# Optimization experiments

Hardware: AMD Instinct MI355X
Metric: run time of the kernel (lower is better)

## Reference

```python
import jax, jax.numpy as jnp
import numpy as np

B, S, H = 2, 2048, 1024
NH, HD = 16, 64
WINDOW = 1024
ROPE_THETA = 10000.0
MAX_POS = 2048


def _rope_tables(dtype=jnp.float32):
    # RotaryEmbedding cache: inv_freq over even dims, emb = cat(freqs, freqs)
    inv_freq = 1.0 / (ROPE_THETA ** (jnp.arange(0, HD, 2, dtype=jnp.float32) / HD))
    t = jnp.arange(MAX_POS, dtype=jnp.float32)
    freqs = jnp.einsum('i,j->ij', t, inv_freq)          # [MAX_POS, HD//2]
    emb = jnp.concatenate([freqs, freqs], axis=-1)      # [MAX_POS, HD]
    return jnp.cos(emb).astype(dtype), jnp.sin(emb).astype(dtype)


def _rotate_half(x):
    x1, x2 = x[..., : HD // 2], x[..., HD // 2:]
    return jnp.concatenate([-x2, x1], axis=-1)


def setup_inputs() -> dict:
    key = jax.random.key(0)
    ks = jax.random.split(key, 5)
    sc = 0.02
    hidden_states = jax.random.normal(ks[0], (B, S, H), dtype=jnp.float32)
    position_ids = jnp.tile(jnp.arange(S, dtype=jnp.int64)[None, :], (B, 1))
    wq = jax.random.normal(ks[1], (H, H), dtype=jnp.float32) * sc
    wk = jax.random.normal(ks[2], (H, H), dtype=jnp.float32) * sc
    wv = jax.random.normal(ks[3], (H, H), dtype=jnp.float32) * sc
    wo = jax.random.normal(ks[4], (H, H), dtype=jnp.float32) * sc
    zeros = jnp.zeros((H,), dtype=jnp.float32)
    return {"hidden_states": hidden_states, "position_ids": position_ids,
            "wq": wq, "bq": zeros, "wk": wk, "bk": zeros,
            "wv": wv, "bv": zeros, "wo": wo, "bo": zeros}


def reference(hidden_states, position_ids, wq, bq, wk, bk, wv, bv, wo, bo):
    b, s, _ = hidden_states.shape
    # projections (nn.Linear: x @ W.T + b), split heads -> [B, NH, S, HD]
    def proj(w, bias):
        y = hidden_states @ w.T + bias
        return y.reshape(b, s, NH, HD).transpose(0, 2, 1, 3)
    q, k, v = proj(wq, bq), proj(wk, bk), proj(wv, bv)

    # RoPE: gather cos/sin at position_ids, broadcast over heads
    cos_t, sin_t = _rope_tables(hidden_states.dtype)
    pos = jnp.clip(position_ids, 0, MAX_POS - 1)
    cos = cos_t[pos][:, None, :, :]   # [B, 1, S, HD]
    sin = sin_t[pos][:, None, :, :]
    q = q * cos + _rotate_half(q) * sin
    k = k * cos + _rotate_half(k) * sin

    # scaled dot-product attention with causal + sliding-window band mask
    scores = jnp.einsum('bhqd,bhkd->bhqk', q, k) / jnp.sqrt(jnp.asarray(HD, hidden_states.dtype))
    i = jnp.arange(s)[:, None]
    j = jnp.arange(s)[None, :]
    allowed = (j <= i) & (i - j < WINDOW)          # banded causal mask [S, S]
    neg = jnp.asarray(jnp.finfo(hidden_states.dtype).min, hidden_states.dtype)
    scores = jnp.where(allowed[None, None, :, :], scores, neg)
    probs = jax.nn.softmax(scores, axis=-1)
    ctx = jnp.einsum('bhqk,bhkd->bhqd', probs, v)  # [B, NH, S, HD]
    ctx = ctx.transpose(0, 2, 1, 3).reshape(b, s, H)
    return ctx @ wo.T + bo
```

## Files before the change

kernel.cpp:

```cpp
#include <hip/hip_runtime.h>

#define BATCH 2
#define SDIM 2048
#define HDIM 1024
#define NHEADS 16
#define HEADD 64
#define WIN 1024

typedef __bf16 bf16x8 __attribute__((ext_vector_type(8)));
typedef __bf16 bf16x4 __attribute__((ext_vector_type(4)));
typedef float f32x4 __attribute__((ext_vector_type(4)));
typedef unsigned short u16x8 __attribute__((ext_vector_type(8)));

__device__ __forceinline__ unsigned short bf16_rne(float f) {
    union { float f; unsigned u; } x; x.f = f;
    unsigned r = x.u + 0x7fffu + ((x.u >> 16) & 1u);
    return (unsigned short)(r >> 16);
}

__device__ __forceinline__ void gload_lds16(const unsigned short* g, unsigned short* l) {
    __builtin_amdgcn_global_load_lds(
        (const __attribute__((address_space(1))) void*)g,
        (__attribute__((address_space(3))) void*)l, 16, 0, 0);
}

__global__ __launch_bounds__(256) void prep_kernel(
    const float* __restrict__ hs, const float* __restrict__ wq, const float* __restrict__ wk,
    const float* __restrict__ wv, const float* __restrict__ wo,
    unsigned short* __restrict__ Xb, unsigned short* __restrict__ Wqkv,
    unsigned short* __restrict__ Wob, float2* __restrict__ cstab)
{
    int i = blockIdx.x * 256 + threadIdx.x;
    if (i < 2097152) {
        const float* src; unsigned short* dst; int off;
        if (i < 1048576)      { src = hs; dst = Xb;             off = i; }
        else if (i < 1310720) { src = wq; dst = Wqkv;           off = i - 1048576; }
        else if (i < 1572864) { src = wk; dst = Wqkv + 1048576; off = i - 1310720; }
        else if (i < 1835008) { src = wv; dst = Wqkv + 2097152; off = i - 1572864; }
        else                  { src = wo; dst = Wob;            off = i - 1835008; }
        float4 v = reinterpret_cast<const float4*>(src)[off];
        ushort4 r;
        r.x = bf16_rne(v.x); r.y = bf16_rne(v.y); r.z = bf16_rne(v.z); r.w = bf16_rne(v.w);
        reinterpret_cast<ushort4*>(dst)[off] = r;
    } else {
        int j = i - 2097152;
        int p = j >> 5, f = j & 31;
        float inv = (float)pow(10000.0, -(double)f / 32.0);
        float ang = (float)p * inv;
        cstab[j] = make_float2(cosf(ang), sinf(ang));
    }
}

__global__ __launch_bounds__(256) void vtrans_kernel(
    const unsigned short* __restrict__ in, unsigned short* __restrict__ out)
{
    __shared__ __align__(16) unsigned short T[64 * 72];
    int s0 = blockIdx.x * 64, h = blockIdx.y, b = blockIdx.z;
    long hb = (long)(b * NHEADS + h) * SDIM * HEADD;
    int t = threadIdx.x;
    int sr = t >> 2, sc = (t & 3) * 16;
    u16x8 v0 = *(const u16x8*)&in[hb + (long)(s0 + sr) * HEADD + sc];
    u16x8 v1 = *(const u16x8*)&in[hb + (long)(s0 + sr) * HEADD + sc + 8];
    #pragma unroll
    for (int j = 0; j < 8; j++) {
        T[(sc + j) * 72     + (sr ^ (sc & 48))] = (unsigned short)v0[j];
        T[(sc + 8 + j) * 72 + (sr ^ (sc & 48))] = (unsigned short)v1[j];
    }
    __syncthreads();
    int dr = t >> 2, dc = (t & 3) * 16;
    int cb = dc ^ (dr & 48);
    u16x8 o0 = *(const u16x8*)&T[dr * 72 + cb];
    u16x8 o1 = *(const u16x8*)&T[dr * 72 + cb + 8];
    *(u16x8*)&out[hb + (long)dr * SDIM + s0 + dc]     = o0;
    *(u16x8*)&out[hb + (long)dr * SDIM + s0 + dc + 8] = o1;
}

__device__ __forceinline__ void mfma_gemm_128(
    const unsigned short* __restrict__ A,
    const unsigned short* __restrict__ Bm,
    int m0, int n0, int tid,
    unsigned short* lA, unsigned short* lB,
    f32x4 acc[4][4])
{
    const int K = 1024;
    const int BUF = 128 * 32;
    int lane = tid & 63, wid = tid >> 6;
    int wm = wid >> 1, wn = wid & 1;
    int lane15 = lane & 15, lhi = lane >> 4;
    int lrow = lane >> 2;
    int swz = (lane & 3) ^ ((lane >> 3) & 3);
    const unsigned short* ga0 = A  + (long)(m0 + wid * 32      + lrow) * K + swz * 8;
    const unsigned short* ga1 = A  + (long)(m0 + wid * 32 + 16 + lrow) * K + swz * 8;
    const unsigned short* gb0 = Bm + (long)(n0 + wid * 32      + lrow) * K + swz * 8;
    const unsigned short* gb1 = Bm + (long)(n0 + wid * 32 + 16 + lrow) * K + swz * 8;
    unsigned short* la0 = lA + (wid * 32)      * 32;
    unsigned short* la1 = lA + (wid * 32 + 16) * 32;
    unsigned short* lb0 = lB + (wid * 32)      * 32;
    unsigned short* lb1 = lB + (wid * 32 + 16) * 32;
    int ru = (lhi ^ ((lane15 >> 1) & 3)) * 8;

#define STAGE_G(boff, kt) \
    gload_lds16(ga0 + (kt) * 32, la0 + (boff)); \
    gload_lds16(ga1 + (kt) * 32, la1 + (boff)); \
    gload_lds16(gb0 + (kt) * 32, lb0 + (boff)); \
    gload_lds16(gb1 + (kt) * 32, lb1 + (boff));

#define COMPUTE_G(off) { \
    bf16x8 af[4], bfr[4]; \
    _Pragma("unroll") \
    for (int f = 0; f < 4; f++) { \
        af[f]  = *(const bf16x8*)&lA[(off) + (wm * 64 + f * 16 + lane15) * 32 + ru]; \
        bfr[f] = *(const bf16x8*)&lB[(off) + (wn * 64 + f * 16 + lane15) * 32 + ru]; \
    } \
    _Pragma("unroll") \
    for (int i = 0; i < 4; i++) \
        _Pragma("unroll") \
        for (int j = 0; j < 4; j++) \
            acc[i][j] = __builtin_amdgcn_mfma_f32_16x16x32_bf16(af[i], bfr[j], acc[i][j], 0, 0, 0); \
}

#define WAITB(n) \
    asm volatile("s_waitcnt vmcnt(" #n ")" ::: "memory"); \
    __builtin_amdgcn_s_barrier(); \
    asm volatile("" ::: "memory");

    STAGE_G(0, 0);
    STAGE_G(BUF, 1);
    #pragma unroll 1
    for (int t = 0; t < 30; t += 3) {
        WAITB(4);
        STAGE_G(2 * BUF, t + 2);
        COMPUTE_G(0);
        WAITB(4);
        STAGE_G(0, t + 3);
        COMPUTE_G(BUF);
        WAITB(4);
        STAGE_G(BUF, t + 4);
        COMPUTE_G(2 * BUF);
    }
    WAITB(4);
    COMPUTE_G(0);
    WAITB(0);
    COMPUTE_G(BUF);

#undef STAGE_G
#undef COMPUTE_G
#undef WAITB
}

__global__ __launch_bounds__(256) void gemm_qkv_kernel(
    const unsigned short* __restrict__ Xb,
    const unsigned short* __restrict__ Wb,
    const float* __restrict__ bq, const float* __restrict__ bk, const float* __restrict__ bv,
    const float2* __restrict__ cstab,
    unsigned short* __restrict__ qbuf, unsigned short* __restrict__ kbuf, unsigned short* __restrict__ vbuf)
{
    __shared__ __align__(16) unsigned short lA[3 * 128 * 32];
    __shared__ __align__(16) unsigned short lB[3 * 128 * 32];
    int tid = threadIdx.x;
    int lane = tid & 63, wid = tid >> 6;
    int wm = wid >> 1, wn = wid & 1;
    int lane15 = lane & 15, lhi = lane >> 4;
    int m0 = blockIdx.y * 128, n0 = blockIdx.x * 128;
    f32x4 acc[4][4];
    #pragma unroll
    for (int i = 0; i < 4; i++)
        #pragma unroll
        for (int j = 0; j < 4; j++)
            acc[i][j] = (f32x4){0.f, 0.f, 0.f, 0.f};

    mfma_gemm_128(Xb, Wb, m0, n0, tid, lA, lB, acc);

    int proj = n0 >> 10;
    int ncol0 = (n0 & 1023) + wn * 64;
    int h = ncol0 >> 6;
    unsigned short* dst = proj == 0 ? qbuf : (proj == 1 ? kbuf : vbuf);
    const float* bias = proj == 0 ? bq : (proj == 1 ? bk : bv);
    #pragma unroll
    for (int fm = 0; fm < 4; fm++) {
        #pragma unroll
        for (int reg = 0; reg < 4; reg++) {
            int m = m0 + wm * 64 + fm * 16 + lhi * 4 + reg;
            int bb = m >> 11, s = m & (SDIM - 1);
            long base = ((long)(bb * NHEADS + h) * SDIM + s) * HEADD;
            if (proj < 2) {
                #pragma unroll
                for (int fn = 0; fn < 2; fn++) {
                    int j = fn * 16 + lane15;
                    float lo = acc[fm][fn][reg]     + bias[ncol0 + j];
                    float hi = acc[fm][fn + 2][reg] + bias[ncol0 + 32 + j];
                    float2 cs = cstab[s * 32 + j];
                    float rl = lo * cs.x - hi * cs.y;
                    float rh = hi * cs.x + lo * cs.y;
                    if (proj == 0) { rl *= 0.125f; rh *= 0.125f; }
                    dst[base + j]      = bf16_rne(rl);
                    dst[base + 32 + j] = bf16_rne(rh);
                }
            } else {
                #pragma unroll
                for (int fn = 0; fn < 4; fn++) {
                    int d = fn * 16 + lane15;
                    dst[base + d] = bf16_rne(acc[fm][fn][reg] + bias[ncol0 + d]);
                }
            }
        }
    }
}

__global__ __launch_bounds__(256) void attn_kernel(
    const unsigned short* __restrict__ qb,
    const unsigned short* __restrict__ kbf,
    const unsigned short* __restrict__ vtb,
    unsigned short* __restrict__ ctxb)
{
    __shared__ __align__(16) unsigned short Kl[64 * 72];
    __shared__ __align__(16) unsigned short Vl[64 * 72];
    __shared__ __align__(16) unsigned short Pl[4][16 * 72];
    int tid = threadIdx.x, lane = tid & 63, wid = tid >> 6;
    int lane15 = lane & 15, lhi = lane >> 4;

    int slot = blockIdx.x;
    int xcd = slot & 7;
    int pos = slot >> 3;
    int hbg = pos >> 5;
    int hb32 = xcd + 8 * hbg;
    int h = hb32 & 15, b = hb32 >> 4;
    int qt = 31 - (pos & 31);
    int q0b = qt * 64;
    int qw = q0b + wid * 16;

    long hb = (long)(b * NHEADS + h) * SDIM * HEADD;
    const unsigned short* qptr = qb + hb;
    const unsigned short* kptr = kbf + hb;
    const unsigned short* vt   = vtb + hb;
    unsigned short* Pw = Pl[wid];

    bf16x8 aq0 = *(const bf16x8*)&qptr[(qw + lane15) * HEADD + lhi * 8];
    bf16x8 aq1 = *(const bf16x8*)&qptr[(qw + lane15) * HEADD + 32 + lhi * 8];

    f32x4 acc[4];
    #pragma unroll
    for (int f = 0; f < 4; f++) acc[f] = (f32x4){0.f, 0.f, 0.f, 0.f};
    float rs = 0.f;

    int t0 = q0b - (WIN - 1);
    int kb0 = t0 > 0 ? (t0 >> 6) : 0;
    int kbl = q0b >> 6;
    int srow = tid >> 2;
    int sc = (tid & 3) * 16;

    u16x8 kr0 = *(const u16x8*)&kptr[(kb0 * 64 + srow) * HEADD + sc];
    u16x8 kr1 = *(const u16x8*)&kptr[(kb0 * 64 + srow) * HEADD + sc + 8];
    u16x8 vr0 = *(const u16x8*)&vt[(long)srow * SDIM + kb0 * 64 + sc];
    u16x8 vr1 = *(const u16x8*)&vt[(long)srow * SDIM + kb0 * 64 + sc + 8];

    for (int kblk = kb0; kblk <= kbl; kblk++) {
        int kbase = kblk * 64;
        __syncthreads();
        *(u16x8*)&Kl[srow * 72 + sc]     = kr0;
        *(u16x8*)&Kl[srow * 72 + sc + 8] = kr1;
        *(u16x8*)&Vl[srow * 72 + sc]     = vr0;
        *(u16x8*)&Vl[srow * 72 + sc + 8] = vr1;
        __syncthreads();
        if (kblk < kbl) {
            int nb = (kblk + 1) * 64;
            kr0 = *(const u16x8*)&kptr[(nb + srow) * HEADD + sc];
            kr1 = *(const u16x8*)&kptr[(nb + srow) * HEADD + sc + 8];
            vr0 = *(const u16x8*)&vt[(long)srow * SDIM + nb + sc];
            vr1 = *(const u16x8*)&vt[(long)srow * SDIM + nb + sc + 8];
        }
        if (kbase + 63 < qw - (WIN - 1)) continue;

        bool full = (kbase + 63 <= qw) && (qw + 15 - kbase < WIN);
        f32x4 S[4];
        #pragma unroll
        for (int fk = 0; fk < 4; fk++) {
            bf16x8 bk0 = *(const bf16x8*)&Kl[(fk * 16 + lane15) * 72 + lhi * 8];
            bf16x8 bk1 = *(const bf16x8*)&Kl[(fk * 16 + lane15) * 72 + 32 + lhi * 8];
            f32x4 s = (f32x4){0.f, 0.f, 0.f, 0.f};
            s = __builtin_amdgcn_mfma_f32_16x16x32_bf16(bk0, aq0, s, 0, 0, 0);
            s = __builtin_amdgcn_mfma_f32_16x16x32_bf16(bk1, aq1, s, 0, 0, 0);
            S[fk] = s;
        }
        if (!full) {
            int q = qw + lane15;
            #pragma unroll
            for (int fk = 0; fk < 4; fk++)
                #pragma unroll
                for (int r = 0; r < 4; r++) {
                    int k = kbase + fk * 16 + lhi * 4 + r;
                    bool ok = (k <= q) && (q - k < WIN);
                    if (!ok) S[fk][r] = -1e30f;
                }
        }
        #pragma unroll
        for (int fk = 0; fk < 4; fk++) {
            bf16x4 c;
            #pragma unroll
            for (int r = 0; r < 4; r++) {
                float p = __expf(S[fk][r]);
                rs += p;
                c[r] = (__bf16)p;
            }
            *(bf16x4*)&Pw[lane15 * 72 + fk * 16 + lhi * 4] = c;
        }
        #pragma unroll
        for (int ks = 0; ks < 2; ks++) {
            bf16x8 pa = *(const bf16x8*)&Pw[lane15 * 72 + ks * 32 + lhi * 8];
            #pragma unroll
            for (int fd = 0; fd < 4; fd++) {
                bf16x8 bv2 = *(const bf16x8*)&Vl[(fd * 16 + lane15) * 72 + ks * 32 + lhi * 8];
                acc[fd] = __builtin_amdgcn_mfma_f32_16x16x32_bf16(pa, bv2, acc[fd], 0, 0, 0);
            }
        }
    }
    rs += __shfl_xor(rs, 16);
    rs += __shfl_xor(rs, 32);
    float linv[4];
    #pragma unroll
    for (int r = 0; r < 4; r++)
        linv[r] = 1.0f / __shfl(rs, lhi * 4 + r);
    #pragma unroll
    for (int fd = 0; fd < 4; fd++)
        #pragma unroll
        for (int r = 0; r < 4; r++) {
            int q = qw + lhi * 4 + r;
            int d = fd * 16 + lane15;
            ctxb[(((long)b * SDIM + q) * NHEADS + h) * HEADD + d] = bf16_rne(acc[fd][r] * linv[r]);
        }
}

__global__ __launch_bounds__(256) void gemm_o_kernel(
    const unsigned short* __restrict__ Ab,
    const unsigned short* __restrict__ Wb,
    const float* __restrict__ bo,
    float* __restrict__ out)
{
    __shared__ __align__(16) unsigned short lA[3 * 128 * 32];
    __shared__ __align__(16) unsigned short lB[3 * 128 * 32];
    int tid = threadIdx.x;
    int lane = tid & 63, wid = tid >> 6;
    int wm = wid >> 1, wn = wid & 1;
    int lane15 = lane & 15, lhi = lane >> 4;
    int m0 = blockIdx.y * 128, n0 = blockIdx.x * 128;
    f32x4 acc[4][4];
    #pragma unroll
    for (int i = 0; i < 4; i++)
        #pragma unroll
        for (int j = 0; j < 4; j++)
            acc[i][j] = (f32x4){0.f, 0.f, 0.f, 0.f};

    mfma_gemm_128(Ab, Wb, m0, n0, tid, lA, lB, acc);

    #pragma unroll
    for (int fm = 0; fm < 4; fm++)
        #pragma unroll
        for (int reg = 0; reg < 4; reg++) {
            int m = m0 + wm * 64 + fm * 16 + lhi * 4 + reg;
            #pragma unroll
            for (int fn = 0; fn < 4; fn++) {
                int n = n0 + wn * 64 + fn * 16 + lane15;
                out[(long)m * HDIM + n] = acc[fm][fn][reg] + bo[n];
            }
        }
}

extern "C" void kernel_launch(void* const* d_in, const int* in_sizes, int n_in,
                              void* d_out, int out_size, void* d_ws, size_t ws_size,
                              hipStream_t stream) {
    const float* hs = (const float*)d_in[0];
    const float* wq = (const float*)d_in[2];
    const float* bq = (const float*)d_in[3];
    const float* wk = (const float*)d_in[4];
    const float* bk = (const float*)d_in[5];
    const float* wv = (const float*)d_in[6];
    const float* bv = (const float*)d_in[7];
    const float* wo = (const float*)d_in[8];
    const float* bo = (const float*)d_in[9];
    float* out = (float*)d_out;

    char* ws = (char*)d_ws;
    unsigned short* Xb    = (unsigned short*)(ws);
    unsigned short* Wqkv  = (unsigned short*)(ws + (8l  << 20));
    unsigned short* Wob   = (unsigned short*)(ws + (14l << 20));
    float2*         cstab = (float2*)        (ws + (16l << 20));
    unsigned short* qbuf  = (unsigned short*)(ws + (17l << 20));
    unsigned short* kbuf  = (unsigned short*)(ws + (25l << 20));
    unsigned short* vbuf  = (unsigned short*)(ws + (33l << 20));
    unsigned short* ctxb  = (unsigned short*)(ws + (41l << 20));
    unsigned short* vT    = Xb;

    prep_kernel<<<8448, 256, 0, stream>>>(hs, wq, wk, wv, wo, Xb, Wqkv, Wob, cstab);
    gemm_qkv_kernel<<<dim3(24, 32), 256, 0, stream>>>(Xb, Wqkv, bq, bk, bv, cstab, qbuf, kbuf, vbuf);
    vtrans_kernel<<<dim3(SDIM / 64, NHEADS, BATCH), 256, 0, stream>>>(vbuf, vT);
    attn_kernel<<<1024, 256, 0, stream>>>(qbuf, kbuf, vT, ctxb);
    gemm_o_kernel<<<dim3(8, 32), 256, 0, stream>>>(ctxb, Wob, bo, out);
}
```

Measured before the change: 118.7 us.

## Enlarge QKV GEMM tiles to 256x256 with 512-thread blocks

```diff
diff --git a/kernel.cpp b/kernel.cpp
--- a/kernel.cpp
+++ b/kernel.cpp
@@ -148,28 +148,89 @@
 #undef WAITB
 }
 
-__global__ __launch_bounds__(256) void gemm_qkv_kernel(
+__global__ __launch_bounds__(512) void gemm_qkv_kernel(
     const unsigned short* __restrict__ Xb,
     const unsigned short* __restrict__ Wb,
     const float* __restrict__ bq, const float* __restrict__ bk, const float* __restrict__ bv,
     const float2* __restrict__ cstab,
     unsigned short* __restrict__ qbuf, unsigned short* __restrict__ kbuf, unsigned short* __restrict__ vbuf)
 {
-    __shared__ __align__(16) unsigned short lA[3 * 128 * 32];
-    __shared__ __align__(16) unsigned short lB[3 * 128 * 32];
+    const int K = 1024;
+    const int BUF = 256 * 32;
+    __shared__ __align__(16) unsigned short lA[3 * 256 * 32];
+    __shared__ __align__(16) unsigned short lB[3 * 256 * 32];
     int tid = threadIdx.x;
     int lane = tid & 63, wid = tid >> 6;
-    int wm = wid >> 1, wn = wid & 1;
+    int wm = wid >> 2, wn = wid & 3;
     int lane15 = lane & 15, lhi = lane >> 4;
-    int m0 = blockIdx.y * 128, n0 = blockIdx.x * 128;
-    f32x4 acc[4][4];
-    #pragma unroll
-    for (int i = 0; i < 4; i++)
+    int m0 = blockIdx.y * 256, n0 = blockIdx.x * 256;
+    int lrow = lane >> 2;
+    int swz = (lane & 3) ^ ((lane >> 3) & 3);
+    const unsigned short* ga0 = Xb + (long)(m0 + wid * 32      + lrow) * K + swz * 8;
+    const unsigned short* ga1 = Xb + (long)(m0 + wid * 32 + 16 + lrow) * K + swz * 8;
+    const unsigned short* gb0 = Wb + (long)(n0 + wid * 32      + lrow) * K + swz * 8;
+    const unsigned short* gb1 = Wb + (long)(n0 + wid * 32 + 16 + lrow) * K + swz * 8;
+    unsigned short* la0 = lA + (wid * 32)      * 32;
+    unsigned short* la1 = lA + (wid * 32 + 16) * 32;
+    unsigned short* lb0 = lB + (wid * 32)      * 32;
+    unsigned short* lb1 = lB + (wid * 32 + 16) * 32;
+    int ru = (lhi ^ ((lane15 >> 1) & 3)) * 8;
+
+    f32x4 acc[8][4];
+    #pragma unroll
+    for (int i = 0; i < 8; i++)
         #pragma unroll
         for (int j = 0; j < 4; j++)
             acc[i][j] = (f32x4){0.f, 0.f, 0.f, 0.f};
 
-    mfma_gemm_128(Xb, Wb, m0, n0, tid, lA, lB, acc);
+#define STAGE_Q(boff, kt) \
+    gload_lds16(ga0 + (kt) * 32, la0 + (boff)); \
+    gload_lds16(ga1 + (kt) * 32, la1 + (boff)); \
+    gload_lds16(gb0 + (kt) * 32, lb0 + (boff)); \
+    gload_lds16(gb1 + (kt) * 32, lb1 + (boff));
+
+#define COMPUTE_Q(off) { \
+    bf16x8 af[8], bfr[4]; \
+    _Pragma("unroll") \
+    for (int f = 0; f < 8; f++) \
+        af[f]  = *(const bf16x8*)&lA[(off) + (wm * 128 + f * 16 + lane15) * 32 + ru]; \
+    _Pragma("unroll") \
+    for (int f = 0; f < 4; f++) \
+        bfr[f] = *(const bf16x8*)&lB[(off) + (wn * 64 + f * 16 + lane15) * 32 + ru]; \
+    _Pragma("unroll") \
+    for (int i = 0; i < 8; i++) \
+        _Pragma("unroll") \
+        for (int j = 0; j < 4; j++) \
+            acc[i][j] = __builtin_amdgcn_mfma_f32_16x16x32_bf16(af[i], bfr[j], acc[i][j], 0, 0, 0); \
+}
+
+#define WAITB(n) \
+    asm volatile("s_waitcnt vmcnt(" #n ")" ::: "memory"); \
+    __builtin_amdgcn_s_barrier(); \
+    asm volatile("" ::: "memory");
+
+    STAGE_Q(0, 0);
+    STAGE_Q(BUF, 1);
+    #pragma unroll 1
+    for (int t = 0; t < 30; t += 3) {
+        WAITB(4);
+        STAGE_Q(2 * BUF, t + 2);
+        COMPUTE_Q(0);
+        WAITB(4);
+        STAGE_Q(0, t + 3);
+        COMPUTE_Q(BUF);
+        WAITB(4);
+        STAGE_Q(BUF, t + 4);
+        COMPUTE_Q(2 * BUF);
+    }
+    WAITB(4);
+    COMPUTE_Q(0);
+    WAITB(0);
+    COMPUTE_Q(BUF);
+
+#undef STAGE_Q
+#undef COMPUTE_Q
+#undef WAITB
 
     int proj = n0 >> 10;
     int ncol0 = (n0 & 1023) + wn * 64;
@@ -177,10 +238,10 @@
     unsigned short* dst = proj == 0 ? qbuf : (proj == 1 ? kbuf : vbuf);
     const float* bias = proj == 0 ? bq : (proj == 1 ? bk : bv);
     #pragma unroll
-    for (int fm = 0; fm < 4; fm++) {
+    for (int fm = 0; fm < 8; fm++) {
         #pragma unroll
         for (int reg = 0; reg < 4; reg++) {
-            int m = m0 + wm * 64 + fm * 16 + lhi * 4 + reg;
+            int m = m0 + wm * 128 + fm * 16 + lhi * 4 + reg;
             int bb = m >> 11, s = m & (SDIM - 1);
             long base = ((long)(bb * NHEADS + h) * SDIM + s) * HEADD;
             if (proj < 2) {
@@ -391,7 +452,7 @@
     unsigned short* vT    = Xb;
 
     prep_kernel<<<8448, 256, 0, stream>>>(hs, wq, wk, wv, wo, Xb, Wqkv, Wob, cstab);
-    gemm_qkv_kernel<<<dim3(24, 32), 256, 0, stream>>>(Xb, Wqkv, bq, bk, bv, cstab, qbuf, kbuf, vbuf);
+    gemm_qkv_kernel<<<dim3(12, 16), 512, 0, stream>>>(Xb, Wqkv, bq, bk, bv, cstab, qbuf, kbuf, vbuf);
     vtrans_kernel<<<dim3(SDIM / 64, NHEADS, BATCH), 256, 0, stream>>>(vbuf, vT);
     attn_kernel<<<1024, 256, 0, stream>>>(qbuf, kbuf, vT, ctxb);
     gemm_o_kernel<<<dim3(8, 32), 256, 0, stream>>>(ctxb, Wob, bo, out);
```

Result: slower. 127.4 us (+7.3%).

## Rewrite QKV GEMM with 256x256 tiles, 512 threads and interleaved staging

Applied to the files above, without the earlier changes.

```diff
diff --git a/kernel.cpp b/kernel.cpp
--- a/kernel.cpp
+++ b/kernel.cpp
@@ -148,28 +148,92 @@
 #undef WAITB
 }
 
-__global__ __launch_bounds__(256) void gemm_qkv_kernel(
+#define BUFE (256 * 64)
+
+#define LDA(C, FM, KK) (*(const bf16x8*)&lA[(C) * BUFE + (wm * 128 + (FM) * 16 + lane15) * 64 + ((((KK) * 4 + lhi) ^ (lane15 & 7)) * 8)])
+#define LDB(C, FN, KK) (*(const bf16x8*)&lB[(C) * BUFE + (wn * 64  + (FN) * 16 + lane15) * 64 + ((((KK) * 4 + lhi) ^ (lane15 & 7)) * 8)])
+#define STGA(C, H, I, KT) gload_lds16(gA + ((H) * 128 + (I) * 8) * 1024 + (KT) * 64, lA + (C) * BUFE + ((H) * 128 + wid * 16 + (I) * 8) * 64)
+#define STGB(C, H, I, KT) gload_lds16(gB + ((H) * 128 + (I) * 8) * 1024 + (KT) * 64, lB + (C) * BUFE + ((H) * 128 + wid * 16 + (I) * 8) * 64)
+
+#define MF(a, b, c) __builtin_amdgcn_mfma_f32_16x16x32_bf16((a), (b), (c), 0, 0, 0)
+
+#define PHASE(C, P, ...) { \
+    bf16x8 x0 = LDA(C, 2 * (P), 0), x1 = LDA(C, 2 * (P), 1); \
+    bf16x8 y0 = LDA(C, 2 * (P) + 1, 0), y1 = LDA(C, 2 * (P) + 1, 1); \
+    __VA_ARGS__ \
+    __builtin_amdgcn_s_setprio(1); \
+    acc[2*(P)][0] = MF(x0, b00, acc[2*(P)][0]); acc[2*(P)][0] = MF(x1, b01, acc[2*(P)][0]); \
+    acc[2*(P)][1] = MF(x0, b10, acc[2*(P)][1]); acc[2*(P)][1] = MF(x1, b11, acc[2*(P)][1]); \
+    acc[2*(P)][2] = MF(x0, b20, acc[2*(P)][2]); acc[2*(P)][2] = MF(x1, b21, acc[2*(P)][2]); \
+    acc[2*(P)][3] = MF(x0, b30, acc[2*(P)][3]); acc[2*(P)][3] = MF(x1, b31, acc[2*(P)][3]); \
+    acc[2*(P)+1][0] = MF(y0, b00, acc[2*(P)+1][0]); acc[2*(P)+1][0] = MF(y1, b01, acc[2*(P)+1][0]); \
+    acc[2*(P)+1][1] = MF(y0, b10, acc[2*(P)+1][1]); acc[2*(P)+1][1] = MF(y1, b11, acc[2*(P)+1][1]); \
+    acc[2*(P)+1][2] = MF(y0, b20, acc[2*(P)+1][2]); acc[2*(P)+1][2] = MF(y1, b21, acc[2*(P)+1][2]); \
+    acc[2*(P)+1][3] = MF(y0, b30, acc[2*(P)+1][3]); acc[2*(P)+1][3] = MF(y1, b31, acc[2*(P)+1][3]); \
+    __builtin_amdgcn_s_setprio(0); }
+
+#define TILEBODY(C, T, SG) { \
+    bf16x8 b00 = LDB(C, 0, 0), b01 = LDB(C, 0, 1), b10 = LDB(C, 1, 0), b11 = LDB(C, 1, 1); \
+    bf16x8 b20 = LDB(C, 2, 0), b21 = LDB(C, 2, 1), b30 = LDB(C, 3, 0), b31 = LDB(C, 3, 1); \
+    PHASE(C, 0, if (SG) { STGA(1 - (C), 1, 0, (T) + 1); STGA(1 - (C), 1, 1, (T) + 1); }) \
+    PHASE(C, 1, if (SG) { STGB(1 - (C), 0, 0, (T) + 1); STGB(1 - (C), 0, 1, (T) + 1); }) \
+    PHASE(C, 2, if (SG) { STGB(1 - (C), 1, 0, (T) + 1); STGB(1 - (C), 1, 1, (T) + 1); }) \
+    PHASE(C, 3, ) }
+
+#define KTILE(CUR, T) \
+    asm volatile("s_waitcnt lgkmcnt(0)" ::: "memory"); \
+    __builtin_amdgcn_s_barrier(); \
+    STGA(1 - (CUR), 0, 0, (T) + 1); STGA(1 - (CUR), 0, 1, (T) + 1); \
+    asm volatile("s_waitcnt vmcnt(2)" ::: "memory"); \
+    __builtin_amdgcn_s_barrier(); \
+    __builtin_amdgcn_sched_barrier(0); \
+    TILEBODY(CUR, T, 1)
+
+__global__ __launch_bounds__(512, 2) void gemm_qkv_kernel(
     const unsigned short* __restrict__ Xb,
     const unsigned short* __restrict__ Wb,
     const float* __restrict__ bq, const float* __restrict__ bk, const float* __restrict__ bv,
     const float2* __restrict__ cstab,
     unsigned short* __restrict__ qbuf, unsigned short* __restrict__ kbuf, unsigned short* __restrict__ vbuf)
 {
-    __shared__ __align__(16) unsigned short lA[3 * 128 * 32];
-    __shared__ __align__(16) unsigned short lB[3 * 128 * 32];
+    __shared__ __align__(16) unsigned short lA[2 * BUFE];
+    __shared__ __align__(16) unsigned short lB[2 * BUFE];
     int tid = threadIdx.x;
     int lane = tid & 63, wid = tid >> 6;
-    int wm = wid >> 1, wn = wid & 1;
+    int wm = wid >> 2, wn = wid & 3;
     int lane15 = lane & 15, lhi = lane >> 4;
-    int m0 = blockIdx.y * 128, n0 = blockIdx.x * 128;
-    f32x4 acc[4][4];
-    #pragma unroll
-    for (int i = 0; i < 4; i++)
+    int bid = blockIdx.x;
+    int sbid = (bid & 7) * 24 + (bid >> 3);
+    int m0 = (sbid / 12) * 256, n0 = (sbid % 12) * 256;
+    int swz8 = (lane & 7) ^ ((lane >> 3) & 7);
+    const unsigned short* gA = Xb + (long)(m0 + wid * 16 + (lane >> 3)) * 1024 + swz8 * 8;
+    const unsigned short* gB = Wb + (long)(n0 + wid * 16 + (lane >> 3)) * 1024 + swz8 * 8;
+
+    f32x4 acc[8][4];
+    #pragma unroll
+    for (int i = 0; i < 8; i++)
         #pragma unroll
         for (int j = 0; j < 4; j++)
             acc[i][j] = (f32x4){0.f, 0.f, 0.f, 0.f};
 
-    mfma_gemm_128(Xb, Wb, m0, n0, tid, lA, lB, acc);
+    STGA(0, 0, 0, 0); STGA(0, 0, 1, 0); STGA(0, 1, 0, 0); STGA(0, 1, 1, 0);
+    STGB(0, 0, 0, 0); STGB(0, 0, 1, 0); STGB(0, 1, 0, 0); STGB(0, 1, 1, 0);
+    STGA(1, 0, 0, 1); STGA(1, 0, 1, 1);
+    asm volatile("s_waitcnt vmcnt(2)" ::: "memory");
+    __builtin_amdgcn_s_barrier();
+    __builtin_amdgcn_sched_barrier(0);
+
+    TILEBODY(0, 0, 1)
+    KTILE(1, 1)   KTILE(0, 2)   KTILE(1, 3)   KTILE(0, 4)
+    KTILE(1, 5)   KTILE(0, 6)   KTILE(1, 7)   KTILE(0, 8)
+    KTILE(1, 9)   KTILE(0, 10)  KTILE(1, 11)  KTILE(0, 12)
+    KTILE(1, 13)  KTILE(0, 14)
+    asm volatile("s_waitcnt lgkmcnt(0)" ::: "memory");
+    __builtin_amdgcn_s_barrier();
+    asm volatile("s_waitcnt vmcnt(0)" ::: "memory");
+    __builtin_amdgcn_s_barrier();
+    __builtin_amdgcn_sched_barrier(0);
+    TILEBODY(1, 15, 0)
 
     int proj = n0 >> 10;
     int ncol0 = (n0 & 1023) + wn * 64;
@@ -177,10 +241,10 @@
     unsigned short* dst = proj == 0 ? qbuf : (proj == 1 ? kbuf : vbuf);
     const float* bias = proj == 0 ? bq : (proj == 1 ? bk : bv);
     #pragma unroll
-    for (int fm = 0; fm < 4; fm++) {
+    for (int fm = 0; fm < 8; fm++) {
         #pragma unroll
         for (int reg = 0; reg < 4; reg++) {
-            int m = m0 + wm * 64 + fm * 16 + lhi * 4 + reg;
+            int m = m0 + wm * 128 + fm * 16 + lhi * 4 + reg;
             int bb = m >> 11, s = m & (SDIM - 1);
             long base = ((long)(bb * NHEADS + h) * SDIM + s) * HEADD;
             if (proj < 2) {
@@ -391,7 +455,7 @@
     unsigned short* vT    = Xb;
 
     prep_kernel<<<8448, 256, 0, stream>>>(hs, wq, wk, wv, wo, Xb, Wqkv, Wob, cstab);
-    gemm_qkv_kernel<<<dim3(24, 32), 256, 0, stream>>>(Xb, Wqkv, bq, bk, bv, cstab, qbuf, kbuf, vbuf);
+    gemm_qkv_kernel<<<192, 512, 0, stream>>>(Xb, Wqkv, bq, bk, bv, cstab, qbuf, kbuf, vbuf);
     vtrans_kernel<<<dim3(SDIM / 64, NHEADS, BATCH), 256, 0, stream>>>(vbuf, vT);
     attn_kernel<<<1024, 256, 0, stream>>>(qbuf, kbuf, vT, ctxb);
     gemm_o_kernel<<<dim3(8, 32), 256, 0, stream>>>(ctxb, Wob, bo, out);
```

New measurement: 117.1 us. About the same (-1.4%).
